# Kernel tuning notes

Measured on AMD Instinct MI355X. Metric: run time of the kernel, lower is better.

The kernel has to match this reference:

```python
import jax, jax.numpy as jnp
import numpy as np

B, T, C = 16, 1023, 2048
N_LAYER, LAYER_ID = 24, 12


def setup_inputs() -> dict:
    key = jax.random.key(0)
    k0, k1, k2, k3, k4 = jax.random.split(key, 5)
    x = jax.random.normal(k0, (B, T, C), jnp.float32)
    # decay schedule exactly as in RWKV_TimeMix.__init__ (first_sa_layer_id = 1)
    f1 = 3.0 + (LAYER_ID - 1) / (N_LAYER - 2) * (1.2 - 3.0)
    f2 = 0.65 + (LAYER_ID - 1) / (N_LAYER - 2) * (0.4 - 0.65)
    h = np.arange(C, dtype=np.float64)
    decay_speed = np.power(f2, h / (C - 1) * 7) * f1
    time_decay = jnp.asarray(np.log(decay_speed), jnp.float32)          # [C]
    time_first = jnp.full((C,), float(np.log(0.3)), jnp.float32)        # [C]
    time_mix = jnp.concatenate([jnp.zeros((C // 2,), jnp.float32),
                                jnp.ones((C - C // 2,), jnp.float32)])  # [C]
    s = 0.02
    Wk = jax.random.normal(k1, (C, C), jnp.float32) * s
    Wv = jax.random.normal(k2, (C, C), jnp.float32) * s
    Wr = jax.random.normal(k3, (C, C), jnp.float32) * s
    Wo = jax.random.normal(k4, (C, C), jnp.float32) * s
    z = jnp.zeros((B, C), jnp.float32)
    return {"x": x, "time_decay": time_decay, "time_first": time_first,
            "time_mix": time_mix, "Wk": Wk, "Wv": Wv, "Wr": Wr, "Wo": Wo,
            "xx": z, "aa": z, "bb": z, "mm": z}


def reference(x, time_decay, time_first, time_mix, Wk, Wv, Wr, Wo, xx, aa, bb, mm):
    Bn, Tn, Cn = x.shape
    # time_shift: prepend carried last-token state xx, drop last
    x_shift = jnp.concatenate([xx[:, None, :], x[:, :-1, :]], axis=1)
    xm = x * time_mix + x_shift * (1.0 - time_mix)
    k = xm @ Wk.T                       # [B, T, C]
    v = xm @ Wv.T
    r = xm @ Wr.T
    # running-max renorm to the nearest power of two: ldexp(0.5, frexp(max_t k).exponent)
    kmax = jax.lax.stop_gradient(jnp.max(k, axis=1))   # [B, C], max over time
    _, expo = jnp.frexp(kmax)
    mm_new = jnp.ldexp(jnp.float32(0.5), expo)          # [B, C]
    k = jnp.exp(k - mm_new[:, None, :])
    kv = k * v
    # TimeX kernel weights: w[c, T-1-delta] = exp(-exp(time_decay[c]) * (delta-1)) = d**(delta-1),
    # w[c, T-1] = exp(time_first[c]); so wk[t] = e_first*k[t] + sum_{u<t} d^{t-1-u} k[u] -> linear scan
    d = jnp.exp(-jnp.exp(time_decay))                   # [C] per-channel decay (= w[...,-3])
    e_first = jnp.exp(time_first)                       # [C] (w[...,-1])
    rsf = jnp.exp(mm - mm_new)                          # rescale carried state to new renorm
    k_seq = jnp.concatenate([(bb * rsf)[:, None, :], k], axis=1)    # [B, T+1, C]
    kv_seq = jnp.concatenate([(aa * rsf)[:, None, :], kv], axis=1)  # [B, T+1, C]

    def step(carry, inp):
        Sk, Skv = carry
        kt, kvt = inp
        out = (e_first * kt + Sk, e_first * kvt + Skv)
        return (d * Sk + kt, d * Skv + kvt), out

    init = (jnp.zeros((Bn, Cn), x.dtype), jnp.zeros((Bn, Cn), x.dtype))
    seq = (jnp.swapaxes(k_seq, 0, 1), jnp.swapaxes(kv_seq, 0, 1))   # [T+1, B, C]
    _, (wk_s, wkv_s) = jax.lax.scan(step, init, seq)
    wk = jnp.swapaxes(wk_s[1:], 0, 1)     # drop state slot -> [B, T, C]
    wkv = jnp.swapaxes(wkv_s[1:], 0, 1)
    rwkv = jax.nn.sigmoid(r) * jnp.nan_to_num(wkv / wk)
    return rwkv @ Wo.T
```

## Files before the change

kernel.cpp:

```cpp
#include <hip/hip_runtime.h>
#include <hip/hip_bf16.h>
#include <hip/hip_fp16.h>
#include <math.h>
#include <float.h>

#define BB 16
#define TT 1023
#define CC 2048
#define M_ROWS (BB * TT)
#define MP 16384
#define N3 (3 * CC)
#define NCH 16
#define CHL 64

typedef __attribute__((ext_vector_type(8))) short bfrag;
typedef __attribute__((ext_vector_type(4))) float f32x4;
typedef __attribute__((ext_vector_type(4))) short short4v;

__device__ __forceinline__ void async16(const void* g, void* l) {
  __builtin_amdgcn_global_load_lds((const __attribute__((address_space(1))) void*)g,
                                   (__attribute__((address_space(3))) void*)l, 16, 0, 0);
}

__device__ __forceinline__ short bfb(float f) {
  __hip_bfloat16 h = __float2bfloat16(f);
  return *reinterpret_cast<short*>(&h);
}

__global__ void prep(const float* __restrict__ x, const float* __restrict__ xx,
                     const float* __restrict__ tmix,
                     const float* __restrict__ Wk, const float* __restrict__ Wv,
                     const float* __restrict__ Wr, const float* __restrict__ Wo,
                     __hip_bfloat16* __restrict__ xm,
                     __hip_bfloat16* __restrict__ W3, __hip_bfloat16* __restrict__ WoB) {
  int bid = blockIdx.x;
  if (bid < MP) {
    int m = bid;
    short* orow = (short*)xm + (size_t)m * CC;
    if (m >= M_ROWS) {
      for (int c = threadIdx.x; c < CC / 4; c += 256)
        ((short4v*)orow)[c] = short4v{0, 0, 0, 0};
      return;
    }
    int b = m / TT, t = m - b * TT;
    const float* xrow = x + (size_t)m * CC;
    const float* xprev = (t == 0) ? (xx + (size_t)b * CC) : (xrow - CC);
    for (int c = threadIdx.x; c < CC / 4; c += 256) {
      float4 xv = ((const float4*)xrow)[c];
      float4 pv = ((const float4*)xprev)[c];
      float4 tm = ((const float4*)tmix)[c];
      ((short4v*)orow)[c] = short4v{
          bfb(xv.x * tm.x + pv.x * (1.0f - tm.x)),
          bfb(xv.y * tm.y + pv.y * (1.0f - tm.y)),
          bfb(xv.z * tm.z + pv.z * (1.0f - tm.z)),
          bfb(xv.w * tm.w + pv.w * (1.0f - tm.w))};
    }
  } else {
    size_t i4 = (size_t)(bid - MP) * 256 + threadIdx.x;
    size_t i = i4 * 4;
    float4 a = *(const float4*)(Wk + i);
    float4 b = *(const float4*)(Wv + i);
    float4 c = *(const float4*)(Wr + i);
    float4 d = *(const float4*)(Wo + i);
    *(short4v*)((short*)W3 + i)               = short4v{bfb(a.x), bfb(a.y), bfb(a.z), bfb(a.w)};
    *(short4v*)((short*)W3 + i + CC * CC)     = short4v{bfb(b.x), bfb(b.y), bfb(b.z), bfb(b.w)};
    *(short4v*)((short*)W3 + i + 2 * CC * CC) = short4v{bfb(c.x), bfb(c.y), bfb(c.z), bfb(c.w)};
    *(short4v*)((short*)WoB + i)              = short4v{bfb(d.x), bfb(d.y), bfb(d.z), bfb(d.w)};
  }
}

template <int MODE>
__global__ __launch_bounds__(512, 2)
void gemm256(const short* __restrict__ A, const short* __restrict__ Bw,
             float* __restrict__ outF, __half* __restrict__ outH,
             __hip_bfloat16* __restrict__ outV, __hip_bfloat16* __restrict__ outR) {
  __shared__ short lds[65536];

  const int lane = threadIdx.x & 63, wid = threadIdx.x >> 6;
  const int wr = wid >> 2, wc = wid & 3;

  const int nx = gridDim.x;
  const int nwg = nx * gridDim.y;
  const int bid = blockIdx.y * nx + blockIdx.x;
  const int q = nwg >> 3;
  const int swz = (bid & 7) * q + (bid >> 3);
  const int mBase = (swz / nx) * 256;
  const int nBase = (swz % nx) * 256;

  const int srow = lane >> 2;
  const int scol = (((lane & 3) ^ ((lane >> 3) & 3)) * 8);
  const int stgOff = wid * 1024 + lane * 8;
  const short* aSrcBase = A  + (size_t)(mBase + wid * 32 + srow) * CC + scol;
  const short* bSrcBase = Bw + (size_t)(nBase + wid * 32 + srow) * CC + scol;

  const int ldOff = (lane & 15) * 32 + (((lane >> 4) ^ ((lane >> 1) & 3)) * 8);

  f32x4 acc[2][4][4] = {};
  bfrag bq[4];

#define RGNA(buf, kh) ((buf) * 32768 + (kh) * 8192)
#define RGNB(buf, kh) (16384 + (buf) * 32768 + (kh) * 8192)

#define STG_A(buf, kh, tk) do { \
    const short* _s = aSrcBase + ((tk) * 64 + (kh) * 32); \
    short* _d = lds + RGNA(buf, kh) + stgOff; \
    async16(_s, _d); async16(_s + (size_t)16 * CC, _d + 512); } while (0)

#define STG_B(buf, kh, tk) do { \
    const short* _s = bSrcBase + ((tk) * 64 + (kh) * 32); \
    short* _d = lds + RGNB(buf, kh) + stgOff; \
    async16(_s, _d); async16(_s + (size_t)16 * CC, _d + 512); } while (0)

#define VMN(n) asm volatile("s_waitcnt vmcnt(" #n ")" ::: "memory")

#define PH(buf, kh, mh, STAGE, WAIT) do { \
    bfrag aq[4]; \
    if ((mh) == 0) { \
      _Pragma("unroll") \
      for (int n = 0; n < 4; ++n) \
        bq[n] = *(const bfrag*)(lds + RGNB(buf, kh) + (wc * 64 + n * 16) * 32 + ldOff); \
    } \
    _Pragma("unroll") \
    for (int f = 0; f < 4; ++f) \
      aq[f] = *(const bfrag*)(lds + RGNA(buf, kh) + (wr * 128 + (mh) * 64 + f * 16) * 32 + ldOff); \
    STAGE; \
    __builtin_amdgcn_s_setprio(1); \
    _Pragma("unroll") \
    for (int f = 0; f < 4; ++f) \
      _Pragma("unroll") \
      for (int n = 0; n < 4; ++n) \
        acc[mh][f][n] = __builtin_amdgcn_mfma_f32_16x16x32_bf16(aq[f], bq[n], acc[mh][f][n], 0, 0, 0); \
    __builtin_amdgcn_s_setprio(0); \
    WAIT; \
    __builtin_amdgcn_s_barrier(); } while (0)

  STG_A(0, 0, 0); STG_B(0, 0, 0);
  STG_A(0, 1, 0); STG_B(0, 1, 0);
  STG_A(1, 0, 1); STG_B(1, 0, 1);
  VMN(4);
  __builtin_amdgcn_s_barrier();

  for (int ti = 0; ti < 30; ti += 2) {
    PH(0, 0, 0, STG_A(1, 1, ti + 1), );
    PH(0, 0, 1, STG_B(1, 1, ti + 1), );
    PH(0, 1, 0, STG_A(0, 0, ti + 2), );
    PH(0, 1, 1, STG_B(0, 0, ti + 2), VMN(4));
    PH(1, 0, 0, STG_A(0, 1, ti + 2), );
    PH(1, 0, 1, STG_B(0, 1, ti + 2), );
    PH(1, 1, 0, STG_A(1, 0, ti + 3), );
    PH(1, 1, 1, STG_B(1, 0, ti + 3), VMN(4));
  }
  PH(0, 0, 0, STG_A(1, 1, 31), );
  PH(0, 0, 1, STG_B(1, 1, 31), );
  PH(0, 1, 0, , );
  PH(0, 1, 1, , VMN(4));
  PH(1, 0, 0, , );
  PH(1, 0, 1, , VMN(0));
  PH(1, 1, 0, , );
  PH(1, 1, 1, , );

#undef PH
#undef VMN
#undef STG_A
#undef STG_B
#undef RGNA
#undef RGNB

#pragma unroll
  for (int mh = 0; mh < 2; ++mh)
#pragma unroll
    for (int f = 0; f < 4; ++f) {
      const int row0 = mBase + wr * 128 + mh * 64 + f * 16 + (lane >> 4) * 4;
      const int col0 = nBase + wc * 64 + (lane & 15);
#pragma unroll
      for (int n = 0; n < 4; ++n) {
        const int col = col0 + n * 16;
#pragma unroll
        for (int rr = 0; rr < 4; ++rr) {
          const int row = row0 + rr;
          if (row < M_ROWS) {
            float val = acc[mh][f][n][rr];
            if constexpr (MODE == 0) {
              outF[(size_t)row * CC + col] = val;
            } else {
              if (col < CC)          outH[(size_t)row * CC + col] = __float2half(expf(val));
              else if (col < 2 * CC) outV[(size_t)row * CC + (col - CC)] = __float2bfloat16(val);
              else                   outR[(size_t)row * CC + (col - 2 * CC)] =
                                         __float2bfloat16(1.0f / (1.0f + expf(-val)));
            }
          }
        }
      }
    }
}

__global__ __launch_bounds__(1024)
void scan_fuse2(const __half* __restrict__ ek, const __hip_bfloat16* __restrict__ v,
                const __hip_bfloat16* __restrict__ sg, const float* __restrict__ aa,
                const float* __restrict__ bb, const float* __restrict__ mm,
                const float* __restrict__ tdec, const float* __restrict__ tfir,
                __hip_bfloat16* __restrict__ rwkv) {
  __shared__ float sBk[NCH][64], sBkv[NCH][64], sSk[NCH][64], sSkv[NCH][64];

  const int lane = threadIdx.x & 63, wid = threadIdx.x >> 6;
  const int c = blockIdx.x * 64 + lane;
  const int b = blockIdx.y;
  const int i = b * CC + c;

  const float dexp = expf(tdec[c]);
  const float d    = expf(-dexp);
  const float ef   = expf(tfir[c]);

  const int t0 = wid * CHL;
  const int t1 = (t0 + CHL < TT) ? t0 + CHL : TT;
  const size_t base = (size_t)b * TT * CC + c;

  if (wid < NCH - 1) {
    float Bk = 0.0f, Bkv = 0.0f;
    size_t off = base + (size_t)t0 * CC;
#pragma unroll 4
    for (int t = t0; t < t1; ++t, off += CC) {
      float kk = __half2float(ek[off]);
      float kv = kk * __bfloat162float(v[off]);
      Bk = d * Bk + kk;
      Bkv = d * Bkv + kv;
    }
    sBk[wid][lane] = Bk;
    sBkv[wid][lane] = Bkv;
  }
  __syncthreads();

  if (wid == 0) {
    const float d64 = expf(-dexp * (float)CHL);
    const float sc = expf(mm[i]);
    float S = bb[i] * sc, Sv = aa[i] * sc;
#pragma unroll
    for (int j = 0; j < NCH; ++j) {
      sSk[j][lane] = S;
      sSkv[j][lane] = Sv;
      if (j < NCH - 1) {
        S = d64 * S + sBk[j][lane];
        Sv = d64 * Sv + sBkv[j][lane];
      }
    }
  }
  __syncthreads();

  float S = sSk[wid][lane], Sv = sSkv[wid][lane];
  size_t off = base + (size_t)t0 * CC;
#pragma unroll 4
  for (int t = t0; t < t1; ++t, off += CC) {
    float kk = __half2float(ek[off]);
    float vv = __bfloat162float(v[off]);
    float sig = __bfloat162float(sg[off]);
    float kv = kk * vv;
    float wk = ef * kk + S;
    float wkv = ef * kv + Sv;
    S = d * S + kk;
    Sv = d * Sv + kv;
    float ratio = wkv / wk;
    if (isnan(ratio)) ratio = 0.0f;
    else if (isinf(ratio)) ratio = ratio > 0.0f ? FLT_MAX : -FLT_MAX;
    rwkv[off] = __float2bfloat16(sig * ratio);
  }
}

extern "C" void kernel_launch(void* const* d_in, const int* in_sizes, int n_in,
                              void* d_out, int out_size, void* d_ws, size_t ws_size,
                              hipStream_t stream) {
  const float* x    = (const float*)d_in[0];
  const float* tdec = (const float*)d_in[1];
  const float* tfir = (const float*)d_in[2];
  const float* tmix = (const float*)d_in[3];
  const float* Wk   = (const float*)d_in[4];
  const float* Wv   = (const float*)d_in[5];
  const float* Wr   = (const float*)d_in[6];
  const float* Wo   = (const float*)d_in[7];
  const float* xx   = (const float*)d_in[8];
  const float* aa   = (const float*)d_in[9];
  const float* bb   = (const float*)d_in[10];
  const float* mm   = (const float*)d_in[11];

  char* ws = (char*)d_ws;
  size_t o = 0;
  __hip_bfloat16* W3  = (__hip_bfloat16*)(ws + o); o += (size_t)N3 * CC * 2;
  __hip_bfloat16* WoB = (__hip_bfloat16*)(ws + o); o += (size_t)CC * CC * 2;
  __hip_bfloat16* xmB = (__hip_bfloat16*)(ws + o); o += (size_t)MP * CC * 2;
  __hip_bfloat16* vB  = (__hip_bfloat16*)(ws + o); o += (size_t)MP * CC * 2;
  __hip_bfloat16* sgB = (__hip_bfloat16*)(ws + o); o += (size_t)MP * CC * 2;

  __half* ekH = (__half*)d_out;
  __hip_bfloat16* rwkvB = xmB;

  prep<<<MP + CC * CC / 1024, 256, 0, stream>>>(x, xx, tmix, Wk, Wv, Wr, Wo,
                                                xmB, W3, WoB);
  gemm256<1><<<dim3(N3 / 256, MP / 256), 512, 0, stream>>>(
      (const short*)xmB, (const short*)W3, nullptr, ekH, vB, sgB);
  scan_fuse2<<<dim3(CC / 64, BB), 1024, 0, stream>>>(ekH, vB, sgB, aa, bb, mm,
                                                     tdec, tfir, rwkvB);
  gemm256<0><<<dim3(CC / 256, MP / 256), 512, 0, stream>>>(
      (const short*)rwkvB, (const short*)WoB, (float*)d_out, nullptr, nullptr, nullptr);
}
```

Baseline: 703.7 us.

## Use 16 waves per GEMM tile and move sigmoid into scan kernel

The 256x256 GEMM tile is now computed by 1024 threads (16 waves in a 4x4 grid), each owning a 64x64 sub-tile instead of 128x64, which halves per-wave accumulators and staging loads and merges the per-half phases into one phase per k-half. This aims to raise latency hiding through more waves per CU, at the cost of more LDS fragment reads per MFMA and more barriers across waves. The sigmoid of r is also moved from the GEMM epilogue into the scan loop, which now stores raw r in bf16.

```diff
diff --git a/kernel.cpp b/kernel.cpp
--- a/kernel.cpp
+++ b/kernel.cpp
@@ -70,7 +70,7 @@
 }
 
 template <int MODE>
-__global__ __launch_bounds__(512, 2)
+__global__ __launch_bounds__(1024, 4)
 void gemm256(const short* __restrict__ A, const short* __restrict__ Bw,
              float* __restrict__ outF, __half* __restrict__ outH,
              __hip_bfloat16* __restrict__ outV, __hip_bfloat16* __restrict__ outR) {
@@ -89,75 +89,60 @@
 
   const int srow = lane >> 2;
   const int scol = (((lane & 3) ^ ((lane >> 3) & 3)) * 8);
-  const int stgOff = wid * 1024 + lane * 8;
-  const short* aSrcBase = A  + (size_t)(mBase + wid * 32 + srow) * CC + scol;
-  const short* bSrcBase = Bw + (size_t)(nBase + wid * 32 + srow) * CC + scol;
+  const int stgOff = wid * 512 + lane * 8;
+  const short* aSrcBase = A  + (size_t)(mBase + wid * 16 + srow) * CC + scol;
+  const short* bSrcBase = Bw + (size_t)(nBase + wid * 16 + srow) * CC + scol;
 
   const int ldOff = (lane & 15) * 32 + (((lane >> 4) ^ ((lane >> 1) & 3)) * 8);
 
-  f32x4 acc[2][4][4] = {};
-  bfrag bq[4];
+  f32x4 acc[4][4] = {};
 
 #define RGNA(buf, kh) ((buf) * 32768 + (kh) * 8192)
 #define RGNB(buf, kh) (16384 + (buf) * 32768 + (kh) * 8192)
 
-#define STG_A(buf, kh, tk) do { \
-    const short* _s = aSrcBase + ((tk) * 64 + (kh) * 32); \
-    short* _d = lds + RGNA(buf, kh) + stgOff; \
-    async16(_s, _d); async16(_s + (size_t)16 * CC, _d + 512); } while (0)
-
-#define STG_B(buf, kh, tk) do { \
-    const short* _s = bSrcBase + ((tk) * 64 + (kh) * 32); \
-    short* _d = lds + RGNB(buf, kh) + stgOff; \
-    async16(_s, _d); async16(_s + (size_t)16 * CC, _d + 512); } while (0)
+#define STG_A(buf, kh, tk) \
+    async16(aSrcBase + ((tk) * 64 + (kh) * 32), lds + RGNA(buf, kh) + stgOff);
+
+#define STG_B(buf, kh, tk) \
+    async16(bSrcBase + ((tk) * 64 + (kh) * 32), lds + RGNB(buf, kh) + stgOff);
 
 #define VMN(n) asm volatile("s_waitcnt vmcnt(" #n ")" ::: "memory")
 
-#define PH(buf, kh, mh, STAGE, WAIT) do { \
-    bfrag aq[4]; \
-    if ((mh) == 0) { \
-      _Pragma("unroll") \
-      for (int n = 0; n < 4; ++n) \
-        bq[n] = *(const bfrag*)(lds + RGNB(buf, kh) + (wc * 64 + n * 16) * 32 + ldOff); \
-    } \
+#define PH(buf, kh, STAGE, WAIT) do { \
+    bfrag aq[4], bq[4]; \
+    _Pragma("unroll") \
+    for (int n = 0; n < 4; ++n) \
+      bq[n] = *(const bfrag*)(lds + RGNB(buf, kh) + (wc * 64 + n * 16) * 32 + ldOff); \
     _Pragma("unroll") \
     for (int f = 0; f < 4; ++f) \
-      aq[f] = *(const bfrag*)(lds + RGNA(buf, kh) + (wr * 128 + (mh) * 64 + f * 16) * 32 + ldOff); \
+      aq[f] = *(const bfrag*)(lds + RGNA(buf, kh) + (wr * 64 + f * 16) * 32 + ldOff); \
     STAGE; \
     __builtin_amdgcn_s_setprio(1); \
     _Pragma("unroll") \
     for (int f = 0; f < 4; ++f) \
       _Pragma("unroll") \
       for (int n = 0; n < 4; ++n) \
-        acc[mh][f][n] = __builtin_amdgcn_mfma_f32_16x16x32_bf16(aq[f], bq[n], acc[mh][f][n], 0, 0, 0); \
+        acc[f][n] = __builtin_amdgcn_mfma_f32_16x16x32_bf16(aq[f], bq[n], acc[f][n], 0, 0, 0); \
     __builtin_amdgcn_s_setprio(0); \
     WAIT; \
     __builtin_amdgcn_s_barrier(); } while (0)
 
-  STG_A(0, 0, 0); STG_B(0, 0, 0);
-  STG_A(0, 1, 0); STG_B(0, 1, 0);
-  STG_A(1, 0, 1); STG_B(1, 0, 1);
-  VMN(4);
+  STG_A(0, 0, 0) STG_B(0, 0, 0)
+  STG_A(0, 1, 0) STG_B(0, 1, 0)
+  STG_A(1, 0, 1) STG_B(1, 0, 1)
+  VMN(2);
   __builtin_amdgcn_s_barrier();
 
   for (int ti = 0; ti < 30; ti += 2) {
-    PH(0, 0, 0, STG_A(1, 1, ti + 1), );
-    PH(0, 0, 1, STG_B(1, 1, ti + 1), );
-    PH(0, 1, 0, STG_A(0, 0, ti + 2), );
-    PH(0, 1, 1, STG_B(0, 0, ti + 2), VMN(4));
-    PH(1, 0, 0, STG_A(0, 1, ti + 2), );
-    PH(1, 0, 1, STG_B(0, 1, ti + 2), );
-    PH(1, 1, 0, STG_A(1, 0, ti + 3), );
-    PH(1, 1, 1, STG_B(1, 0, ti + 3), VMN(4));
-  }
-  PH(0, 0, 0, STG_A(1, 1, 31), );
-  PH(0, 0, 1, STG_B(1, 1, 31), );
-  PH(0, 1, 0, , );
-  PH(0, 1, 1, , VMN(4));
-  PH(1, 0, 0, , );
-  PH(1, 0, 1, , VMN(0));
-  PH(1, 1, 0, , );
-  PH(1, 1, 1, , );
+    PH(0, 0, STG_A(1, 1, ti + 1) STG_B(1, 1, ti + 1), );
+    PH(0, 1, STG_A(0, 0, ti + 2) STG_B(0, 0, ti + 2), VMN(2));
+    PH(1, 0, STG_A(0, 1, ti + 2) STG_B(0, 1, ti + 2), );
+    PH(1, 1, STG_A(1, 0, ti + 3) STG_B(1, 0, ti + 3), VMN(2));
+  }
+  PH(0, 0, STG_A(1, 1, 31) STG_B(1, 1, 31), );
+  PH(0, 1, , VMN(2));
+  PH(1, 0, , VMN(0));
+  PH(1, 1, , );
 
 #undef PH
 #undef VMN
@@ -167,36 +152,33 @@
 #undef RGNB
 
 #pragma unroll
-  for (int mh = 0; mh < 2; ++mh)
-#pragma unroll
-    for (int f = 0; f < 4; ++f) {
-      const int row0 = mBase + wr * 128 + mh * 64 + f * 16 + (lane >> 4) * 4;
-      const int col0 = nBase + wc * 64 + (lane & 15);
-#pragma unroll
-      for (int n = 0; n < 4; ++n) {
-        const int col = col0 + n * 16;
-#pragma unroll
-        for (int rr = 0; rr < 4; ++rr) {
-          const int row = row0 + rr;
-          if (row < M_ROWS) {
-            float val = acc[mh][f][n][rr];
-            if constexpr (MODE == 0) {
-              outF[(size_t)row * CC + col] = val;
-            } else {
-              if (col < CC)          outH[(size_t)row * CC + col] = __float2half(expf(val));
-              else if (col < 2 * CC) outV[(size_t)row * CC + (col - CC)] = __float2bfloat16(val);
-              else                   outR[(size_t)row * CC + (col - 2 * CC)] =
-                                         __float2bfloat16(1.0f / (1.0f + expf(-val)));
-            }
+  for (int f = 0; f < 4; ++f) {
+    const int row0 = mBase + wr * 64 + f * 16 + (lane >> 4) * 4;
+    const int col0 = nBase + wc * 64 + (lane & 15);
+#pragma unroll
+    for (int n = 0; n < 4; ++n) {
+      const int col = col0 + n * 16;
+#pragma unroll
+      for (int rr = 0; rr < 4; ++rr) {
+        const int row = row0 + rr;
+        if (row < M_ROWS) {
+          float val = acc[f][n][rr];
+          if constexpr (MODE == 0) {
+            outF[(size_t)row * CC + col] = val;
+          } else {
+            if (col < CC)          outH[(size_t)row * CC + col] = __float2half(expf(val));
+            else if (col < 2 * CC) outV[(size_t)row * CC + (col - CC)] = __float2bfloat16(val);
+            else                   outR[(size_t)row * CC + (col - 2 * CC)] = __float2bfloat16(val);
           }
         }
       }
     }
+  }
 }
 
 __global__ __launch_bounds__(1024)
 void scan_fuse2(const __half* __restrict__ ek, const __hip_bfloat16* __restrict__ v,
-                const __hip_bfloat16* __restrict__ sg, const float* __restrict__ aa,
+                const __hip_bfloat16* __restrict__ r, const float* __restrict__ aa,
                 const float* __restrict__ bb, const float* __restrict__ mm,
                 const float* __restrict__ tdec, const float* __restrict__ tfir,
                 __hip_bfloat16* __restrict__ rwkv) {
@@ -252,7 +234,7 @@
   for (int t = t0; t < t1; ++t, off += CC) {
     float kk = __half2float(ek[off]);
     float vv = __bfloat162float(v[off]);
-    float sig = __bfloat162float(sg[off]);
+    float rv = __bfloat162float(r[off]);
     float kv = kk * vv;
     float wk = ef * kk + S;
     float wkv = ef * kv + Sv;
@@ -261,6 +243,7 @@
     float ratio = wkv / wk;
     if (isnan(ratio)) ratio = 0.0f;
     else if (isinf(ratio)) ratio = ratio > 0.0f ? FLT_MAX : -FLT_MAX;
+    float sig = 1.0f / (1.0f + expf(-rv));
     rwkv[off] = __float2bfloat16(sig * ratio);
   }
 }
@@ -287,17 +270,17 @@
   __hip_bfloat16* WoB = (__hip_bfloat16*)(ws + o); o += (size_t)CC * CC * 2;
   __hip_bfloat16* xmB = (__hip_bfloat16*)(ws + o); o += (size_t)MP * CC * 2;
   __hip_bfloat16* vB  = (__hip_bfloat16*)(ws + o); o += (size_t)MP * CC * 2;
-  __hip_bfloat16* sgB = (__hip_bfloat16*)(ws + o); o += (size_t)MP * CC * 2;
+  __hip_bfloat16* rB  = (__hip_bfloat16*)(ws + o); o += (size_t)MP * CC * 2;
 
   __half* ekH = (__half*)d_out;
   __hip_bfloat16* rwkvB = xmB;
 
   prep<<<MP + CC * CC / 1024, 256, 0, stream>>>(x, xx, tmix, Wk, Wv, Wr, Wo,
                                                 xmB, W3, WoB);
-  gemm256<1><<<dim3(N3 / 256, MP / 256), 512, 0, stream>>>(
-      (const short*)xmB, (const short*)W3, nullptr, ekH, vB, sgB);
-  scan_fuse2<<<dim3(CC / 64, BB), 1024, 0, stream>>>(ekH, vB, sgB, aa, bb, mm,
+  gemm256<1><<<dim3(N3 / 256, MP / 256), 1024, 0, stream>>>(
+      (const short*)xmB, (const short*)W3, nullptr, ekH, vB, rB);
+  scan_fuse2<<<dim3(CC / 64, BB), 1024, 0, stream>>>(ekH, vB, rB, aa, bb, mm,
                                                      tdec, tfir, rwkvB);
-  gemm256<0><<<dim3(CC / 256, MP / 256), 512, 0, stream>>>(
+  gemm256<0><<<dim3(CC / 256, MP / 256), 1024, 0, stream>>>(
       (const short*)rwkvB, (const short*)WoB, (float*)d_out, nullptr, nullptr, nullptr);
 }
```

After: 676.7 us (median of 2 runs). -3.8%, faster.
